# Optimization experiments

Hardware: AMD Instinct MI355X
Metric: run time of the kernel (lower is better)

The kernel has to match this reference:

```python
import jax, jax.numpy as jnp
import numpy as np

N = 100000  # num nodes
E = 3200000  # num edges (before self-loops)


def setup_inputs() -> dict:
    key = jax.random.key(0)
    k1, k2, k3, k4 = jax.random.split(key, 4)
    x = jax.random.normal(k1, (N, 128), dtype=jnp.float32)
    edge_index = jax.random.randint(k2, (2, E), 0, N, dtype=jnp.int64)
    W1 = jax.random.normal(k3, (128, 64), dtype=jnp.float32) * (1.0 / np.sqrt(128))
    b1 = jnp.zeros((64,), dtype=jnp.float32)
    W2 = jax.random.normal(k4, (64, 1), dtype=jnp.float32) * (1.0 / np.sqrt(64))
    b2 = jnp.zeros((1,), dtype=jnp.float32)
    return {"x": x, "edge_index": edge_index, "W1": W1, "b1": b1, "W2": W2, "b2": b2}


def _gcn_norm(edge_index, num_nodes):
    # add self-loops, then symmetric normalization deg^-1/2[row]*deg^-1/2[col]
    loops = jnp.arange(num_nodes, dtype=edge_index.dtype)
    row = jnp.concatenate([edge_index[0], loops])  # destination
    col = jnp.concatenate([edge_index[1], loops])  # source
    deg = jax.ops.segment_sum(jnp.ones_like(row, dtype=jnp.float32), row,
                              num_segments=num_nodes)
    dinv = jnp.where(deg > 0, jax.lax.rsqrt(deg), 0.0)
    norm = dinv[row] * dinv[col]  # [E+N]
    return row, col, norm


def _gcn_conv(x, row, col, norm, W, b, num_nodes):
    h = x @ W                                   # transform before propagate
    msg = h[col] * norm[:, None]                # gather + scale  [E+N, out]
    out = jax.ops.segment_sum(msg, row, num_segments=num_nodes)  # scatter-add
    return out + b


def reference(x, edge_index, W1, b1, W2, b2):
    row, col, norm = _gcn_norm(edge_index, N)
    h = _gcn_conv(x, row, col, norm, W1, b1, N)
    h = jax.nn.relu(h)
    # dropout p=0.0 -> identity
    h = _gcn_conv(h, row, col, norm, W2, b2, N)
    return jax.nn.sigmoid(h)
```

## Files before the change

kernel.cpp:

```cpp
#include <hip/hip_runtime.h>
#include <hip/hip_bf16.h>
#include <math.h>

#define BKT_SHIFT 8
#define BKT_W     256
#define NBP       512
#define CHUNK     8192
#define CAPR      9216
#define CAPC      10240

__global__ void init_k(const unsigned* __restrict__ e, int* __restrict__ flag,
                       int* __restrict__ bcur, int nb) {
  int t = blockIdx.x * blockDim.x + threadIdx.x;
  if (t == 0) {
    int z = (e[1] == 0u) + (e[3] == 0u) + (e[5] == 0u) + (e[7] == 0u);
    *flag = (z == 4) ? 1 : 0;
  }
  if (t < nb) bcur[t] = t * CAPR;
}

__global__ __launch_bounds__(512) void bin_k(const void* __restrict__ ei, int* __restrict__ bcur,
                                             unsigned* __restrict__ recs, const int* __restrict__ flag,
                                             int E, int NB) {
  __shared__ unsigned srec[CHUNK];
  __shared__ int h[NBP], scex[NBP], cur[NBP], gb[NBP], s[NBP];
  int t = threadIdx.x;
  h[t] = 0;
  __syncthreads();
  bool f64 = (*flag) != 0;
  int start = blockIdx.x * CHUNK;
  int cntE = min(CHUNK, E - start);
  int r[16], c[16];
#pragma unroll
  for (int j = 0; j < 16; ++j) {
    int i = t + j * 512;
    int e = start + min(i, cntE - 1);
    if (f64) {
      r[j] = (int)((const long long*)ei)[e];
      c[j] = (int)((const long long*)ei)[(long long)E + e];
    } else {
      r[j] = ((const int*)ei)[e];
      c[j] = ((const int*)ei)[E + e];
    }
    if (i < cntE) atomicAdd(&h[r[j] >> BKT_SHIFT], 1);
  }
  __syncthreads();
  int v = h[t];
  s[t] = v;
  __syncthreads();
  for (int d = 1; d < NBP; d <<= 1) {
    int a = (t >= d) ? s[t - d] : 0;
    __syncthreads();
    s[t] += a;
    __syncthreads();
  }
  scex[t] = s[t] - v;
  cur[t] = s[t] - v;
  __syncthreads();
  if (t < NB && v) gb[t] = atomicAdd(&bcur[t], v);
#pragma unroll
  for (int j = 0; j < 16; ++j) {
    int i = t + j * 512;
    if (i < cntE) {
      int b = r[j] >> BKT_SHIFT;
      int slot = atomicAdd(&cur[b], 1);
      srec[slot] = ((unsigned)(r[j] & (BKT_W - 1)) << 17) | (unsigned)c[j];
    }
  }
  __syncthreads();
  for (int i = t; i < cntE; i += 512) {
    int lo = 0, hi = NB - 1;
    while (lo < hi) { int mid = (lo + hi + 1) >> 1; if (scex[mid] <= i) lo = mid; else hi = mid - 1; }
    recs[gb[lo] + (i - scex[lo])] = srec[i];
  }
}

__global__ __launch_bounds__(256) void csr_k(const unsigned* __restrict__ recs,
                                             const int* __restrict__ bcur,
                                             int* __restrict__ csr, int* __restrict__ offs,
                                             int* __restrict__ degs, float* __restrict__ dinv, int N) {
  __shared__ unsigned colbuf[CAPC];
  __shared__ int cnt[BKT_W], scx[BKT_W], cur[BKT_W], tmp[BKT_W];
  __shared__ int wtot;
  int t = threadIdx.x;
  int b = blockIdx.x;
  int rbase = b * CAPR;
  int size = min(bcur[b] - rbase, CAPR);
  int cbase = b * CAPC;
  int nb0 = b << BKT_SHIFT;
  int nNodes = min(BKT_W, N - nb0);
  cnt[t] = 0;
  __syncthreads();
  for (int i = t; i < size; i += 256) atomicAdd(&cnt[recs[rbase + i] >> 17], 1);
  __syncthreads();
  int seg = (cnt[t] + 3) & ~3;
  tmp[t] = seg;
  __syncthreads();
  for (int d = 1; d < BKT_W; d <<= 1) {
    int a = (t >= d) ? tmp[t - d] : 0;
    __syncthreads();
    tmp[t] += a;
    __syncthreads();
  }
  scx[t] = tmp[t] - seg;
  cur[t] = tmp[t] - seg;
  if (t == BKT_W - 1) wtot = tmp[t];
  __syncthreads();
  for (int i = t; i < size; i += 256) {
    unsigned rec = recs[rbase + i];
    int lr = rec >> 17;
    int slot = atomicAdd(&cur[lr], 1);
    colbuf[slot] = rec & 0x1FFFFu;
  }
  __syncthreads();
  int wt = wtot;
  for (int i = t; i < wt; i += 256) csr[cbase + i] = colbuf[i];
  if (t < nNodes) {
    offs[nb0 + t] = cbase + scx[t];
    degs[nb0 + t] = cnt[t];
    dinv[nb0 + t] = rsqrtf((float)(cnt[t] + 1));
  }
}

__device__ __forceinline__ unsigned short f2bs(float v) {
  __hip_bfloat16 b = __float2bfloat16(v);
  return *reinterpret_cast<unsigned short*>(&b);
}

__global__ __launch_bounds__(256) void gemm_k(const float* __restrict__ x,
                                              const float* __restrict__ W1,
                                              const float* __restrict__ dinv,
                                              __hip_bfloat16* __restrict__ q, int n) {
  __shared__ float4 xs[64 * 32];
  __shared__ float4 ws[64 * 16];
  int t = threadIdx.x;
  int row0 = blockIdx.x * 64;
  const float4* xg = (const float4*)x;
  const float4* wg = (const float4*)W1;
#pragma unroll
  for (int i = 0; i < 8; ++i) {
    int flat = t + i * 256;
    int r = flat >> 5, c = flat & 31;
    int gr = min(row0 + r, n - 1);
    xs[r * 32 + (c ^ (r & 31))] = xg[(size_t)gr * 32 + c];
  }
  int c4g = t & 15;
  int r4g = t >> 4;
  float acc[4][4];
#pragma unroll
  for (int j = 0; j < 4; ++j)
#pragma unroll
    for (int cc = 0; cc < 4; ++cc) acc[j][cc] = 0.f;
#pragma unroll
  for (int h = 0; h < 2; ++h) {
    if (h) __syncthreads();
#pragma unroll
    for (int i = 0; i < 4; ++i) {
      int flat = t + i * 256;
      ws[flat] = wg[(h * 64 + (flat >> 4)) * 16 + (flat & 15)];
    }
    __syncthreads();
#pragma unroll 2
    for (int k4 = 0; k4 < 16; ++k4) {
      float4 xv[4], wv[4];
#pragma unroll
      for (int j = 0; j < 4; ++j) {
        int r = r4g * 4 + j;
        xv[j] = xs[r * 32 + ((h * 16 + k4) ^ (r & 31))];
      }
#pragma unroll
      for (int kk = 0; kk < 4; ++kk) wv[kk] = ws[(k4 * 4 + kk) * 16 + c4g];
#pragma unroll
      for (int j = 0; j < 4; ++j) {
        acc[j][0] = fmaf(xv[j].x, wv[0].x, acc[j][0]);
        acc[j][1] = fmaf(xv[j].x, wv[0].y, acc[j][1]);
        acc[j][2] = fmaf(xv[j].x, wv[0].z, acc[j][2]);
        acc[j][3] = fmaf(xv[j].x, wv[0].w, acc[j][3]);
        acc[j][0] = fmaf(xv[j].y, wv[1].x, acc[j][0]);
        acc[j][1] = fmaf(xv[j].y, wv[1].y, acc[j][1]);
        acc[j][2] = fmaf(xv[j].y, wv[1].z, acc[j][2]);
        acc[j][3] = fmaf(xv[j].y, wv[1].w, acc[j][3]);
        acc[j][0] = fmaf(xv[j].z, wv[2].x, acc[j][0]);
        acc[j][1] = fmaf(xv[j].z, wv[2].y, acc[j][1]);
        acc[j][2] = fmaf(xv[j].z, wv[2].z, acc[j][2]);
        acc[j][3] = fmaf(xv[j].z, wv[2].w, acc[j][3]);
        acc[j][0] = fmaf(xv[j].w, wv[3].x, acc[j][0]);
        acc[j][1] = fmaf(xv[j].w, wv[3].y, acc[j][1]);
        acc[j][2] = fmaf(xv[j].w, wv[3].z, acc[j][2]);
        acc[j][3] = fmaf(xv[j].w, wv[3].w, acc[j][3]);
      }
    }
  }
#pragma unroll
  for (int j = 0; j < 4; ++j) {
    int r = row0 + r4g * 4 + j;
    if (r < n) {
      float di = dinv[r];
      ushort4 o;
      o.x = f2bs(di * acc[j][0]);
      o.y = f2bs(di * acc[j][1]);
      o.z = f2bs(di * acc[j][2]);
      o.w = f2bs(di * acc[j][3]);
      ((uint2*)q)[(size_t)r * 16 + c4g] = *reinterpret_cast<uint2*>(&o);
    }
  }
}

__device__ __forceinline__ float bflo(unsigned u) { return __uint_as_float(u << 16); }
__device__ __forceinline__ float bfhi(unsigned u) { return __uint_as_float(u & 0xFFFF0000u); }

__global__ __launch_bounds__(256) void agg1_k(const __hip_bfloat16* __restrict__ q,
                                              const int* __restrict__ offs,
                                              const int* __restrict__ degs,
                                              const int* __restrict__ csr,
                                              const float* __restrict__ dinv,
                                              const float* __restrict__ b1,
                                              const float* __restrict__ W2,
                                              float* __restrict__ p, int n) {
  int lane = threadIdx.x & 63;
  int node = blockIdx.x * 4 + (threadIdx.x >> 6);
  if (node >= n) return;
  int grp = lane >> 3;
  int fl = lane & 7;
  int o0 = offs[node];
  int deg = degs[node];
  const uint4* qrows = (const uint4*)q;
  float acc[8] = {0.f, 0.f, 0.f, 0.f, 0.f, 0.f, 0.f, 0.f};
  for (int base = 0; base < deg; base += 32) {
    int e4 = base + grp * 4;
    int4 idx = *(const int4*)(csr + o0 + e4);
    int cc0 = (e4 + 0 < deg) ? idx.x : 0;
    int cc1 = (e4 + 1 < deg) ? idx.y : 0;
    int cc2 = (e4 + 2 < deg) ? idx.z : 0;
    int cc3 = (e4 + 3 < deg) ? idx.w : 0;
    float w0 = (e4 + 0 < deg) ? 1.f : 0.f;
    float w1 = (e4 + 1 < deg) ? 1.f : 0.f;
    float w2 = (e4 + 2 < deg) ? 1.f : 0.f;
    float w3 = (e4 + 3 < deg) ? 1.f : 0.f;
    uint4 v0 = qrows[(size_t)cc0 * 8 + fl];
    uint4 v1 = qrows[(size_t)cc1 * 8 + fl];
    uint4 v2 = qrows[(size_t)cc2 * 8 + fl];
    uint4 v3 = qrows[(size_t)cc3 * 8 + fl];
    acc[0] = fmaf(w0, bflo(v0.x), acc[0]); acc[1] = fmaf(w0, bfhi(v0.x), acc[1]);
    acc[2] = fmaf(w0, bflo(v0.y), acc[2]); acc[3] = fmaf(w0, bfhi(v0.y), acc[3]);
    acc[4] = fmaf(w0, bflo(v0.z), acc[4]); acc[5] = fmaf(w0, bfhi(v0.z), acc[5]);
    acc[6] = fmaf(w0, bflo(v0.w), acc[6]); acc[7] = fmaf(w0, bfhi(v0.w), acc[7]);
    acc[0] = fmaf(w1, bflo(v1.x), acc[0]); acc[1] = fmaf(w1, bfhi(v1.x), acc[1]);
    acc[2] = fmaf(w1, bflo(v1.y), acc[2]); acc[3] = fmaf(w1, bfhi(v1.y), acc[3]);
    acc[4] = fmaf(w1, bflo(v1.z), acc[4]); acc[5] = fmaf(w1, bfhi(v1.z), acc[5]);
    acc[6] = fmaf(w1, bflo(v1.w), acc[6]); acc[7] = fmaf(w1, bfhi(v1.w), acc[7]);
    acc[0] = fmaf(w2, bflo(v2.x), acc[0]); acc[1] = fmaf(w2, bfhi(v2.x), acc[1]);
    acc[2] = fmaf(w2, bflo(v2.y), acc[2]); acc[3] = fmaf(w2, bfhi(v2.y), acc[3]);
    acc[4] = fmaf(w2, bflo(v2.z), acc[4]); acc[5] = fmaf(w2, bfhi(v2.z), acc[5]);
    acc[6] = fmaf(w2, bflo(v2.w), acc[6]); acc[7] = fmaf(w2, bfhi(v2.w), acc[7]);
    acc[0] = fmaf(w3, bflo(v3.x), acc[0]); acc[1] = fmaf(w3, bfhi(v3.x), acc[1]);
    acc[2] = fmaf(w3, bflo(v3.y), acc[2]); acc[3] = fmaf(w3, bfhi(v3.y), acc[3]);
    acc[4] = fmaf(w3, bflo(v3.z), acc[4]); acc[5] = fmaf(w3, bfhi(v3.z), acc[5]);
    acc[6] = fmaf(w3, bflo(v3.w), acc[6]); acc[7] = fmaf(w3, bfhi(v3.w), acc[7]);
  }
#pragma unroll
  for (int j = 0; j < 8; ++j) {
    acc[j] += __shfl_xor(acc[j], 8);
    acc[j] += __shfl_xor(acc[j], 16);
    acc[j] += __shfl_xor(acc[j], 32);
  }
  uint4 vs = qrows[(size_t)node * 8 + fl];
  float qs[8] = {bflo(vs.x), bfhi(vs.x), bflo(vs.y), bfhi(vs.y),
                 bflo(vs.z), bfhi(vs.z), bflo(vs.w), bfhi(vs.w)};
  float di = dinv[node];
  float4 bb0 = ((const float4*)b1)[fl * 2], bb1 = ((const float4*)b1)[fl * 2 + 1];
  float4 ww0 = ((const float4*)W2)[fl * 2], ww1 = ((const float4*)W2)[fl * 2 + 1];
  float bbv[8] = {bb0.x, bb0.y, bb0.z, bb0.w, bb1.x, bb1.y, bb1.z, bb1.w};
  float w2v[8] = {ww0.x, ww0.y, ww0.z, ww0.w, ww1.x, ww1.y, ww1.z, ww1.w};
  float tacc = 0.f;
#pragma unroll
  for (int j = 0; j < 8; ++j)
    tacc += fmaxf(fmaf(di, acc[j] + qs[j], bbv[j]), 0.f) * w2v[j];
  tacc += __shfl_xor(tacc, 1); tacc += __shfl_xor(tacc, 2); tacc += __shfl_xor(tacc, 4);
  if (lane == 0) p[node] = di * tacc;
}

__global__ __launch_bounds__(256) void agg2_k(const float* __restrict__ p,
                                              const int* __restrict__ offs,
                                              const int* __restrict__ degs,
                                              const int* __restrict__ csr,
                                              const float* __restrict__ dinv,
                                              const float* __restrict__ b2,
                                              float* __restrict__ out, int n) {
  int lane = threadIdx.x & 63;
  int node = blockIdx.x * 4 + (threadIdx.x >> 6);
  if (node >= n) return;
  int o0 = offs[node];
  int dg = degs[node];
  float s = 0.f;
  for (int e = lane; e < dg; e += 64) s += p[csr[o0 + e]];
  s += __shfl_xor(s, 1); s += __shfl_xor(s, 2); s += __shfl_xor(s, 4);
  s += __shfl_xor(s, 8); s += __shfl_xor(s, 16); s += __shfl_xor(s, 32);
  if (lane == 0) {
    float z = fmaf(dinv[node], s + p[node], b2[0]);
    out[node] = 1.f / (1.f + expf(-z));
  }
}

extern "C" void kernel_launch(void* const* d_in, const int* in_sizes, int n_in,
                              void* d_out, int out_size, void* d_ws, size_t ws_size,
                              hipStream_t stream) {
  const float* x  = (const float*)d_in[0];
  const void*  ei = d_in[1];
  const float* W1 = (const float*)d_in[2];
  const float* b1 = (const float*)d_in[3];
  const float* W2 = (const float*)d_in[4];
  const float* b2 = (const float*)d_in[5];
  float* out = (float*)d_out;
  const int N = in_sizes[0] / 128;
  const int E = in_sizes[1] / 2;
  const int NB = (N + BKT_W - 1) >> BKT_SHIFT;
  const int nchunks = (E + CHUNK - 1) / CHUNK;
  (void)n_in; (void)out_size; (void)ws_size;

  char* base = (char*)d_ws;
  size_t off = 0;
  auto alloc = [&](size_t bytes) -> void* {
    void* ptr = base + off;
    off += (bytes + 1023) & ~(size_t)1023;
    return ptr;
  };
  int*   flag = (int*)alloc(64);
  int*   bcur = (int*)alloc((size_t)NBP * 4);
  int*   offs = (int*)alloc((size_t)N * 4);
  int*   degs = (int*)alloc((size_t)N * 4);
  float* dinv = (float*)alloc((size_t)N * 4);
  unsigned* recs = (unsigned*)alloc((size_t)NB * CAPR * 4);
  int*   csr  = (int*)alloc((size_t)NB * CAPC * 4);
  __hip_bfloat16* q = (__hip_bfloat16*)alloc((size_t)N * 64 * 2);
  float* p    = (float*)alloc((size_t)N * 4);

  init_k<<<1, 512, 0, stream>>>((const unsigned*)ei, flag, bcur, NBP);
  bin_k<<<nchunks, 512, 0, stream>>>(ei, bcur, recs, flag, E, NB);
  csr_k<<<NB, 256, 0, stream>>>(recs, bcur, csr, offs, degs, dinv, N);
  gemm_k<<<(N + 63) / 64, 256, 0, stream>>>(x, W1, dinv, q, N);
  agg1_k<<<(N + 3) / 4, 256, 0, stream>>>(q, offs, degs, csr, dinv, b1, W2, p, N);
  agg2_k<<<(N + 3) / 4, 256, 0, stream>>>(p, offs, degs, csr, dinv, b2, out, N);
}
```

Before: 168.2 us.

## Rewrite layer-1 aggregation as lane-per-feature persistent waves with padded CSR

CSR segments are now padded to multiples of 8 and filled with a sentinel index pointing at an extra zero row of q, so the gather loop needs no bounds masking. agg1_k becomes a grid-stride persistent kernel where each lane owns one feature and edge indices are broadcast with readlane, issuing 2-byte gathers per lane instead of 16-byte vector loads across lane groups. This removes the per-edge predication and the cross-group shuffle reduction. In exchange it adds padding work and more memory, and the narrow per-lane loads may coalesce less efficiently.

```diff
diff --git a/kernel.cpp b/kernel.cpp
--- a/kernel.cpp
+++ b/kernel.cpp
@@ -7,7 +7,7 @@
 #define NBP       512
 #define CHUNK     8192
 #define CAPR      9216
-#define CAPC      10240
+#define CAPC      11264
 
 __global__ void init_k(const unsigned* __restrict__ e, int* __restrict__ flag,
                        int* __restrict__ bcur, int nb) {
@@ -93,7 +93,8 @@
   __syncthreads();
   for (int i = t; i < size; i += 256) atomicAdd(&cnt[recs[rbase + i] >> 17], 1);
   __syncthreads();
-  int seg = (cnt[t] + 3) & ~3;
+  int myc = cnt[t];
+  int seg = (myc + 7) & ~7;
   tmp[t] = seg;
   __syncthreads();
   for (int d = 1; d < BKT_W; d <<= 1) {
@@ -112,13 +113,14 @@
     int slot = atomicAdd(&cur[lr], 1);
     colbuf[slot] = rec & 0x1FFFFu;
   }
+  for (int i = scx[t] + myc; i < scx[t] + seg; ++i) colbuf[i] = (unsigned)N;
   __syncthreads();
   int wt = wtot;
   for (int i = t; i < wt; i += 256) csr[cbase + i] = colbuf[i];
   if (t < nNodes) {
     offs[nb0 + t] = cbase + scx[t];
-    degs[nb0 + t] = cnt[t];
-    dinv[nb0 + t] = rsqrtf((float)(cnt[t] + 1));
+    degs[nb0 + t] = myc;
+    dinv[nb0 + t] = rsqrtf((float)(myc + 1));
   }
 }
 
@@ -202,12 +204,11 @@
       o.z = f2bs(di * acc[j][2]);
       o.w = f2bs(di * acc[j][3]);
       ((uint2*)q)[(size_t)r * 16 + c4g] = *reinterpret_cast<uint2*>(&o);
-    }
-  }
-}
-
-__device__ __forceinline__ float bflo(unsigned u) { return __uint_as_float(u << 16); }
-__device__ __forceinline__ float bfhi(unsigned u) { return __uint_as_float(u & 0xFFFF0000u); }
+    } else if (r == n) {
+      ((uint2*)q)[(size_t)r * 16 + c4g] = make_uint2(0u, 0u);
+    }
+  }
+}
 
 __global__ __launch_bounds__(256) void agg1_k(const __hip_bfloat16* __restrict__ q,
                                               const int* __restrict__ offs,
@@ -218,66 +219,42 @@
                                               const float* __restrict__ W2,
                                               float* __restrict__ p, int n) {
   int lane = threadIdx.x & 63;
-  int node = blockIdx.x * 4 + (threadIdx.x >> 6);
-  if (node >= n) return;
-  int grp = lane >> 3;
-  int fl = lane & 7;
-  int o0 = offs[node];
-  int deg = degs[node];
-  const uint4* qrows = (const uint4*)q;
-  float acc[8] = {0.f, 0.f, 0.f, 0.f, 0.f, 0.f, 0.f, 0.f};
-  for (int base = 0; base < deg; base += 32) {
-    int e4 = base + grp * 4;
-    int4 idx = *(const int4*)(csr + o0 + e4);
-    int cc0 = (e4 + 0 < deg) ? idx.x : 0;
-    int cc1 = (e4 + 1 < deg) ? idx.y : 0;
-    int cc2 = (e4 + 2 < deg) ? idx.z : 0;
-    int cc3 = (e4 + 3 < deg) ? idx.w : 0;
-    float w0 = (e4 + 0 < deg) ? 1.f : 0.f;
-    float w1 = (e4 + 1 < deg) ? 1.f : 0.f;
-    float w2 = (e4 + 2 < deg) ? 1.f : 0.f;
-    float w3 = (e4 + 3 < deg) ? 1.f : 0.f;
-    uint4 v0 = qrows[(size_t)cc0 * 8 + fl];
-    uint4 v1 = qrows[(size_t)cc1 * 8 + fl];
-    uint4 v2 = qrows[(size_t)cc2 * 8 + fl];
-    uint4 v3 = qrows[(size_t)cc3 * 8 + fl];
-    acc[0] = fmaf(w0, bflo(v0.x), acc[0]); acc[1] = fmaf(w0, bfhi(v0.x), acc[1]);
-    acc[2] = fmaf(w0, bflo(v0.y), acc[2]); acc[3] = fmaf(w0, bfhi(v0.y), acc[3]);
-    acc[4] = fmaf(w0, bflo(v0.z), acc[4]); acc[5] = fmaf(w0, bfhi(v0.z), acc[5]);
-    acc[6] = fmaf(w0, bflo(v0.w), acc[6]); acc[7] = fmaf(w0, bfhi(v0.w), acc[7]);
-    acc[0] = fmaf(w1, bflo(v1.x), acc[0]); acc[1] = fmaf(w1, bfhi(v1.x), acc[1]);
-    acc[2] = fmaf(w1, bflo(v1.y), acc[2]); acc[3] = fmaf(w1, bfhi(v1.y), acc[3]);
-    acc[4] = fmaf(w1, bflo(v1.z), acc[4]); acc[5] = fmaf(w1, bfhi(v1.z), acc[5]);
-    acc[6] = fmaf(w1, bflo(v1.w), acc[6]); acc[7] = fmaf(w1, bfhi(v1.w), acc[7]);
-    acc[0] = fmaf(w2, bflo(v2.x), acc[0]); acc[1] = fmaf(w2, bfhi(v2.x), acc[1]);
-    acc[2] = fmaf(w2, bflo(v2.y), acc[2]); acc[3] = fmaf(w2, bfhi(v2.y), acc[3]);
-    acc[4] = fmaf(w2, bflo(v2.z), acc[4]); acc[5] = fmaf(w2, bfhi(v2.z), acc[5]);
-    acc[6] = fmaf(w2, bflo(v2.w), acc[6]); acc[7] = fmaf(w2, bfhi(v2.w), acc[7]);
-    acc[0] = fmaf(w3, bflo(v3.x), acc[0]); acc[1] = fmaf(w3, bfhi(v3.x), acc[1]);
-    acc[2] = fmaf(w3, bflo(v3.y), acc[2]); acc[3] = fmaf(w3, bfhi(v3.y), acc[3]);
-    acc[4] = fmaf(w3, bflo(v3.z), acc[4]); acc[5] = fmaf(w3, bfhi(v3.z), acc[5]);
-    acc[6] = fmaf(w3, bflo(v3.w), acc[6]); acc[7] = fmaf(w3, bfhi(v3.w), acc[7]);
-  }
-#pragma unroll
-  for (int j = 0; j < 8; ++j) {
-    acc[j] += __shfl_xor(acc[j], 8);
-    acc[j] += __shfl_xor(acc[j], 16);
-    acc[j] += __shfl_xor(acc[j], 32);
-  }
-  uint4 vs = qrows[(size_t)node * 8 + fl];
-  float qs[8] = {bflo(vs.x), bfhi(vs.x), bflo(vs.y), bfhi(vs.y),
-                 bflo(vs.z), bfhi(vs.z), bflo(vs.w), bfhi(vs.w)};
-  float di = dinv[node];
-  float4 bb0 = ((const float4*)b1)[fl * 2], bb1 = ((const float4*)b1)[fl * 2 + 1];
-  float4 ww0 = ((const float4*)W2)[fl * 2], ww1 = ((const float4*)W2)[fl * 2 + 1];
-  float bbv[8] = {bb0.x, bb0.y, bb0.z, bb0.w, bb1.x, bb1.y, bb1.z, bb1.w};
-  float w2v[8] = {ww0.x, ww0.y, ww0.z, ww0.w, ww1.x, ww1.y, ww1.z, ww1.w};
-  float tacc = 0.f;
-#pragma unroll
-  for (int j = 0; j < 8; ++j)
-    tacc += fmaxf(fmaf(di, acc[j] + qs[j], bbv[j]), 0.f) * w2v[j];
-  tacc += __shfl_xor(tacc, 1); tacc += __shfl_xor(tacc, 2); tacc += __shfl_xor(tacc, 4);
-  if (lane == 0) p[node] = di * tacc;
+  int wave = blockIdx.x * 4 + (threadIdx.x >> 6);
+  int nw = gridDim.x * 4;
+  float b1v = b1[lane];
+  float w2v = W2[lane];
+  const unsigned short* qs = (const unsigned short*)q;
+  for (int node = wave; node < n; node += nw) {
+    int ns = __builtin_amdgcn_readfirstlane(node);
+    int o0 = offs[ns];
+    int dg = degs[ns];
+    int dgp = (dg + 7) & ~7;
+    float acc = 0.f;
+    for (int b0 = 0; b0 < dgp; b0 += 64) {
+      int rem = dgp - b0;
+      int mm = rem < 64 ? rem : 64;
+      int idx = n;
+      if (lane < mm) idx = csr[o0 + b0 + lane];
+      for (int e = 0; e < mm; e += 8) {
+        float v[8];
+#pragma unroll
+        for (int k = 0; k < 8; ++k) {
+          int c = __builtin_amdgcn_readlane(idx, e + k);
+          const unsigned short* qp = qs + ((size_t)(unsigned)c << 6);
+          v[k] = __uint_as_float(((unsigned)qp[lane]) << 16);
+        }
+#pragma unroll
+        for (int k = 0; k < 8; ++k) acc += v[k];
+      }
+    }
+    float selfv = __uint_as_float(((unsigned)qs[((size_t)(unsigned)ns << 6) + lane]) << 16);
+    float di = dinv[ns];
+    float h = fmaf(di, acc + selfv, b1v);
+    float tt = fmaxf(h, 0.f) * w2v;
+    tt += __shfl_xor(tt, 1);  tt += __shfl_xor(tt, 2);  tt += __shfl_xor(tt, 4);
+    tt += __shfl_xor(tt, 8);  tt += __shfl_xor(tt, 16); tt += __shfl_xor(tt, 32);
+    if (lane == 0) p[ns] = di * tt;
+  }
 }
 
 __global__ __launch_bounds__(256) void agg2_k(const float* __restrict__ p,
@@ -332,13 +309,13 @@
   float* dinv = (float*)alloc((size_t)N * 4);
   unsigned* recs = (unsigned*)alloc((size_t)NB * CAPR * 4);
   int*   csr  = (int*)alloc((size_t)NB * CAPC * 4);
-  __hip_bfloat16* q = (__hip_bfloat16*)alloc((size_t)N * 64 * 2);
+  __hip_bfloat16* q = (__hip_bfloat16*)alloc(((size_t)N + 1) * 64 * 2);
   float* p    = (float*)alloc((size_t)N * 4);
 
   init_k<<<1, 512, 0, stream>>>((const unsigned*)ei, flag, bcur, NBP);
   bin_k<<<nchunks, 512, 0, stream>>>(ei, bcur, recs, flag, E, NB);
   csr_k<<<NB, 256, 0, stream>>>(recs, bcur, csr, offs, degs, dinv, N);
-  gemm_k<<<(N + 63) / 64, 256, 0, stream>>>(x, W1, dinv, q, N);
-  agg1_k<<<(N + 3) / 4, 256, 0, stream>>>(q, offs, degs, csr, dinv, b1, W2, p, N);
+  gemm_k<<<(N + 64) / 64, 256, 0, stream>>>(x, W1, dinv, q, N);
+  agg1_k<<<2048, 256, 0, stream>>>(q, offs, degs, csr, dinv, b1, W2, p, N);
   agg2_k<<<(N + 3) / 4, 256, 0, stream>>>(p, offs, degs, csr, dinv, b2, out, N);
 }
```

New measurement: 170.4 us. About the same (+1.3%).
